# Kernel optimization log

Measured on AMD Instinct MI355X. Metric: run time of the kernel, lower is better.

The kernel has to match this reference:

```python
import jax, jax.numpy as jnp
import numpy as np

IMG = 64
STEPS = 10
UNITS = 256
PATCH_DIM = (IMG // 2) * (IMG // 2) * 9  # 3x3 patches, stride 2, SAME
ENC_IN = PATCH_DIM + 2 * UNITS  # read_window (patch+h_dec) concat h_dec again


def lstm_cell(x, h, c, kernel, rec, bias):
    # Keras LSTMCell gate order: i, f, g(candidate), o
    z = x @ kernel + h @ rec + bias
    i, f, g, o = jnp.split(z, 4, axis=-1)
    c_new = jax.nn.sigmoid(f) * c + jax.nn.sigmoid(i) * jnp.tanh(g)
    h_new = jax.nn.sigmoid(o) * jnp.tanh(c_new)
    return h_new, c_new


def extract_patches(img):
    # img: [B, H, W] -> 3x3 patches, stride 2, SAME -> [B, (H/2)*(W/2)*9]
    p = jax.lax.conv_general_dilated_patches(
        img[:, None, :, :], (3, 3), (2, 2), 'SAME')  # [B, 9, H/2, W/2]
    p = jnp.transpose(p, (0, 2, 3, 1))  # TF extract_patches layout [B,H',W',9]
    return p.reshape(img.shape[0], -1)


def setup_inputs() -> dict:
    key = jax.random.key(0)
    ks = jax.random.split(key, 8)
    B = 512
    s = 0.05  # small init scale to avoid gate saturation
    return {
        'x': jax.random.uniform(ks[0], (B, IMG, IMG), dtype=jnp.float32),
        'enc_kernel': jax.random.normal(ks[1], (ENC_IN, 4 * UNITS), dtype=jnp.float32) * s,
        'enc_rec': jax.random.normal(ks[2], (UNITS, 4 * UNITS), dtype=jnp.float32) * s,
        'enc_bias': jnp.zeros((4 * UNITS,), jnp.float32),
        'dec_kernel': jax.random.normal(ks[3], (UNITS, 4 * UNITS), dtype=jnp.float32) * s,
        'dec_rec': jax.random.normal(ks[4], (UNITS, 4 * UNITS), dtype=jnp.float32) * s,
        'dec_bias': jnp.zeros((4 * UNITS,), jnp.float32),
        'W_enc': jax.random.normal(ks[5], (UNITS, 10), dtype=jnp.float32) * s,
        'b_enc': jnp.zeros((10,), jnp.float32),
        'W_dec': jax.random.normal(ks[6], (UNITS, IMG * IMG), dtype=jnp.float32) * s,
        'b_dec': jnp.zeros((IMG * IMG,), jnp.float32),
    }


def reference(x, enc_kernel, enc_rec, enc_bias, dec_kernel, dec_rec, dec_bias,
              W_enc, b_enc, W_dec, b_dec):
    B = x.shape[0]
    canvas0 = jnp.zeros((B, IMG, IMG), x.dtype)
    h_enc0 = c_enc0 = h_dec0 = c_dec0 = jnp.zeros((B, UNITS), x.dtype)

    def step(carry, _):
        canvas, h_enc, c_enc, h_dec, c_dec = carry
        x_hat = x - jax.nn.sigmoid(canvas)                      # error image
        patches = extract_patches(x_hat)                        # [B, PATCH_DIM]
        read_window = jnp.concatenate([patches, h_dec], axis=1)
        enc_in = jnp.concatenate([read_window, h_dec], axis=1)  # [B, ENC_IN]
        h_enc, c_enc = lstm_cell(enc_in, h_enc, c_enc, enc_kernel, enc_rec, enc_bias)
        # attention over 10 slots; glimpse vector as attn-weighted slot embeddings
        attn = jax.nn.softmax(h_enc @ W_enc + b_enc, axis=1)    # [B, 10]
        z = attn @ W_enc.T                                      # [B, UNITS]
        h_dec, c_dec = lstm_cell(z, h_dec, c_dec, dec_kernel, dec_rec, dec_bias)
        canvas = canvas + (h_dec @ W_dec + b_dec).reshape(B, IMG, IMG)
        return (canvas, h_enc, c_enc, h_dec, c_dec), None

    (canvas, _, _, _, _), _ = jax.lax.scan(
        step, (canvas0, h_enc0, c_enc0, h_dec0, c_dec0), None, length=STEPS)
    return canvas
```

## Files before the change

### kernel.cpp

```cpp
#include <hip/hip_runtime.h>

typedef unsigned short ushort_t;
typedef __attribute__((ext_vector_type(8))) short short8;
typedef __attribute__((ext_vector_type(4))) float floatx4;

#define BSZ   512
#define UNITS 256
#define IMG   64
#define STEPS 10
#define GATES 1024
#define KENC  4608
#define ESPLIT 8
#define DSPLIT 4

__device__ inline float b2f(ushort_t u) {
  union { float f; unsigned int i; } v; v.i = ((unsigned int)u) << 16; return v.f;
}
__device__ inline ushort_t f2b(float f) {
  unsigned int u = __float_as_uint(f);
  u += 0x7fffu + ((u >> 16) & 1u);
  return (ushort_t)(u >> 16);
}
__device__ inline float sigm(float x) { return 1.f / (1.f + __expf(-x)); }

#define GLL(g, l) __builtin_amdgcn_global_load_lds(                      \
    (const __attribute__((address_space(1))) void*)(g),                  \
    (__attribute__((address_space(3))) void*)(l), 16, 0, 0)

__global__ __launch_bounds__(256) void k_prep_pix(const float* __restrict__ ek,
                                                  ushort_t* __restrict__ ohi) {
  __shared__ float T[64][68];
  int t = threadIdx.x;
  int pix0 = blockIdx.x * 64, n0 = blockIdx.y * 64;
  int r = t >> 2, seg = t & 3;
  int pix = pix0 + r;
  int ri = pix >> 6, ci = pix & 63;
  float4 acc4[4];
#pragma unroll
  for (int j = 0; j < 4; ++j) acc4[j] = float4{0.f, 0.f, 0.f, 0.f};
#pragma unroll
  for (int di = 0; di < 3; ++di) {
    int ii = ri - di;
    if (ii < 0 || (ii & 1)) continue;
    int oi = ii >> 1;  if (oi >= 32) continue;
#pragma unroll
    for (int dj = 0; dj < 3; ++dj) {
      int jj = ci - dj;
      if (jj < 0 || (jj & 1)) continue;
      int oj = jj >> 1;  if (oj >= 32) continue;
      const float* row = ek + (size_t)((oi * 32 + oj) * 9 + di * 3 + dj) * GATES
                         + n0 + seg * 16;
#pragma unroll
      for (int j = 0; j < 4; ++j) {
        float4 v = *(const float4*)(row + j * 4);
        acc4[j].x += v.x; acc4[j].y += v.y; acc4[j].z += v.z; acc4[j].w += v.w;
      }
    }
  }
#pragma unroll
  for (int j = 0; j < 4; ++j) *(float4*)&T[r][seg * 16 + j * 4] = acc4[j];
  __syncthreads();
  ushort_t thi[16];
#pragma unroll
  for (int j = 0; j < 16; ++j) thi[j] = f2b(T[seg * 16 + j][r]);
  size_t off = (size_t)(n0 + r) * KENC + pix0 + seg * 16;
  *(uint4*)(ohi + off)     = *(const uint4*)&thi[0];
  *(uint4*)(ohi + off + 8) = *(const uint4*)&thi[8];
}

__global__ __launch_bounds__(256) void k_prep_multi(
    const float* __restrict__ ek, const float* __restrict__ er,
    const float* __restrict__ dk, const float* __restrict__ dr,
    const float* __restrict__ Wdec,
    ushort_t* __restrict__ Wet_hi,
    ushort_t* __restrict__ Wdt_hi, ushort_t* __restrict__ Wdt_lo,
    ushort_t* __restrict__ Wct_hi, ushort_t* __restrict__ Wct_lo) {
  __shared__ float T[64][68];
  int t = threadIdx.x;
  int z = blockIdx.z;
  int k0 = blockIdx.x * 64, n0 = blockIdx.y * 64;
  int r = t >> 2, seg = t & 3;

  const float *s0, *s1 = nullptr;
  ushort_t *ohi, *olo = nullptr;
  int src_ld, out_ld, koff;
  if (z == 0) { s0 = ek + (size_t)9216 * GATES; s1 = ek + (size_t)9472 * GATES;
                src_ld = GATES; ohi = Wet_hi; out_ld = KENC; koff = 4096; }
  else if (z == 1) { s0 = er; src_ld = GATES; ohi = Wet_hi; out_ld = KENC; koff = 4352; }
  else if (z == 2) { s0 = dk; src_ld = GATES; ohi = Wdt_hi; olo = Wdt_lo; out_ld = 512; koff = 0; }
  else if (z == 3) { s0 = dr; src_ld = GATES; ohi = Wdt_hi; olo = Wdt_lo; out_ld = 512; koff = 256; }
  else { s0 = Wdec; src_ld = 4096; ohi = Wct_hi; olo = Wct_lo; out_ld = 256; koff = 0;
         n0 += (z - 4) * 1024; }

  const float* src = s0 + (size_t)(k0 + r) * src_ld + n0 + seg * 16;
  const float* src2 = s1 ? (s1 + (size_t)(k0 + r) * src_ld + n0 + seg * 16) : nullptr;
#pragma unroll
  for (int j = 0; j < 4; ++j) {
    float4 v = *(const float4*)(src + j * 4);
    if (src2) {
      float4 w = *(const float4*)(src2 + j * 4);
      v.x += w.x; v.y += w.y; v.z += w.z; v.w += w.w;
    }
    *(float4*)&T[r][seg * 16 + j * 4] = v;
  }
  __syncthreads();
  ushort_t thi[16], tlo[16];
#pragma unroll
  for (int j = 0; j < 16; ++j) {
    float v = T[seg * 16 + j][r];
    ushort_t h = f2b(v);
    thi[j] = h;
    tlo[j] = f2b(v - b2f(h));
  }
  size_t off = (size_t)(n0 + r) * out_ld + koff + k0 + seg * 16;
  *(uint4*)(ohi + off)     = *(const uint4*)&thi[0];
  *(uint4*)(ohi + off + 8) = *(const uint4*)&thi[8];
  if (olo) {
    *(uint4*)(olo + off)     = *(const uint4*)&tlo[0];
    *(uint4*)(olo + off + 8) = *(const uint4*)&tlo[8];
  }
}

__global__ __launch_bounds__(256) void k_init(float* __restrict__ canvas,
                                              float* __restrict__ c_enc,
                                              float* __restrict__ c_dec,
                                              ushort_t* __restrict__ ehi,
                                              ushort_t* __restrict__ dhi,
                                              ushort_t* __restrict__ dlo) {
  int b = blockIdx.x, u = threadIdx.x;
  int gid = b * 256 + u;
  float4* cv4 = (float4*)canvas;
#pragma unroll
  for (int j = 0; j < 4; ++j) cv4[gid + j * 131072] = float4{0.f, 0.f, 0.f, 0.f};
  c_enc[gid] = 0.f; c_dec[gid] = 0.f;
  ehi[(size_t)b * KENC + 4096 + u] = 0; ehi[(size_t)b * KENC + 4352 + u] = 0;
  dhi[(size_t)b * 512 + u] = 0; dhi[(size_t)b * 512 + 256 + u] = 0;
  dlo[(size_t)b * 512 + u] = 0; dlo[(size_t)b * 512 + 256 + u] = 0;
}

__global__ __launch_bounds__(256) void k_xhat0(const float* __restrict__ x,
                                               ushort_t* __restrict__ ehi) {
  int tid = blockIdx.x * 256 + threadIdx.x;
  int b = tid >> 12, pix = tid & 4095;
  ehi[(size_t)b * KENC + pix] = f2b(x[tid] - 0.5f);
}

#define TM 128
#define TN 128
#define BK 32

__global__ __launch_bounds__(512, 2) void gemm_e1(
    const ushort_t* __restrict__ Ahi, int lda,
    const ushort_t* __restrict__ Bhi, int ldbt,
    float* __restrict__ C, int ldc, int kiters) {
  __shared__ ushort_t ls[2][2][TM * BK];
  int t = threadIdx.x;
  int m0 = blockIdx.y * TM, n0 = blockIdx.x * TN;
  int z = blockIdx.z;
  int kstart = z * kiters * BK;
  int lane = t & 63, w = t >> 6;
  int wm = w >> 1, wn = w & 1;
  int q = lane >> 4, c16 = lane & 15;

  const ushort_t* pAh = Ahi + (size_t)(m0 + (t >> 2)) * lda + kstart + (t & 3) * 8;
  const ushort_t* pBh = Bhi + (size_t)(n0 + (t >> 2)) * ldbt + kstart + (t & 3) * 8;
  const int d0 = t * 8;

  floatx4 acc[2][4];
#pragma unroll
  for (int i = 0; i < 2; ++i)
#pragma unroll
    for (int j = 0; j < 4; ++j) acc[i][j] = floatx4{0.f, 0.f, 0.f, 0.f};

  GLL(pAh, &ls[0][0][d0]); GLL(pBh, &ls[0][1][d0]);
  pAh += BK; pBh += BK;
  __syncthreads();

  for (int kt = 0; kt < kiters; ++kt) {
    int cur = kt & 1, nxt = cur ^ 1;
    if (kt + 1 < kiters) {
      GLL(pAh, &ls[nxt][0][d0]); GLL(pBh, &ls[nxt][1][d0]);
      pAh += BK; pBh += BK;
    }
    short8 ah[2], bh[4];
#pragma unroll
    for (int i = 0; i < 2; ++i) {
      int ra = (wm * 32 + i * 16 + c16) * BK + q * 8;
      ah[i] = *(const short8*)&ls[cur][0][ra];
    }
#pragma unroll
    for (int j = 0; j < 4; ++j) {
      int rb = (wn * 64 + j * 16 + c16) * BK + q * 8;
      bh[j] = *(const short8*)&ls[cur][1][rb];
    }
#pragma unroll
    for (int mi = 0; mi < 2; ++mi)
#pragma unroll
      for (int ni = 0; ni < 4; ++ni)
        acc[mi][ni] = __builtin_amdgcn_mfma_f32_16x16x32_bf16(ah[mi], bh[ni], acc[mi][ni], 0, 0, 0);
    __syncthreads();
  }

  float* Cz = C + (size_t)z * BSZ * ldc;
#pragma unroll
  for (int mi = 0; mi < 2; ++mi)
#pragma unroll
    for (int ni = 0; ni < 4; ++ni) {
      int n = n0 + wn * 64 + ni * 16 + c16;
      int mb = m0 + wm * 32 + mi * 16 + q * 4;
#pragma unroll
      for (int r = 0; r < 4; ++r)
        Cz[(size_t)(mb + r) * ldc + n] = acc[mi][ni][r];
    }
}

__global__ __launch_bounds__(512, 2) void gemm_d(
    const ushort_t* __restrict__ Ahi, const ushort_t* __restrict__ Alo, int lda,
    const ushort_t* __restrict__ Bhi, const ushort_t* __restrict__ Blo, int ldbt,
    float* __restrict__ C, int ldc, int kiters) {
  __shared__ ushort_t ls[2][12288];
  int t = threadIdx.x;
  int m0 = blockIdx.y * TM, n0 = blockIdx.x * 64;
  int z = blockIdx.z;
  int kstart = z * kiters * BK;
  int lane = t & 63, w = t >> 6;
  int wm = w >> 1, wn = w & 1;
  int q = lane >> 4, c16 = lane & 15;
  int ta = t & 255;

  const ushort_t* pAh = Ahi + (size_t)(m0 + (t >> 2)) * lda + kstart + (t & 3) * 8;
  const ushort_t* pAl = Alo + (size_t)(m0 + (t >> 2)) * lda + kstart + (t & 3) * 8;
  const ushort_t* pB = ((t < 256) ? Bhi : Blo)
                       + (size_t)(n0 + (ta >> 2)) * ldbt + kstart + (ta & 3) * 8;
  const int dAh = t * 8, dAl = 4096 + t * 8;
  const int dB = ((t < 256) ? 8192 : 10240) + ta * 8;

  floatx4 acc[2][2];
#pragma unroll
  for (int i = 0; i < 2; ++i)
#pragma unroll
    for (int j = 0; j < 2; ++j) acc[i][j] = floatx4{0.f, 0.f, 0.f, 0.f};

  GLL(pAh, &ls[0][dAh]); GLL(pAl, &ls[0][dAl]); GLL(pB, &ls[0][dB]);
  pAh += BK; pAl += BK; pB += BK;
  __syncthreads();

  for (int kt = 0; kt < kiters; ++kt) {
    int cur = kt & 1, nxt = cur ^ 1;
    if (kt + 1 < kiters) {
      GLL(pAh, &ls[nxt][dAh]); GLL(pAl, &ls[nxt][dAl]); GLL(pB, &ls[nxt][dB]);
      pAh += BK; pAl += BK; pB += BK;
    }
    short8 ah[2], al[2], bh[2], bl[2];
#pragma unroll
    for (int i = 0; i < 2; ++i) {
      int ra = (wm * 32 + i * 16 + c16) * BK + q * 8;
      ah[i] = *(const short8*)&ls[cur][ra];
      al[i] = *(const short8*)&ls[cur][4096 + ra];
      int rb = (wn * 32 + i * 16 + c16) * BK + q * 8;
      bh[i] = *(const short8*)&ls[cur][8192 + rb];
      bl[i] = *(const short8*)&ls[cur][10240 + rb];
    }
#pragma unroll
    for (int mi = 0; mi < 2; ++mi)
#pragma unroll
      for (int ni = 0; ni < 2; ++ni) {
        acc[mi][ni] = __builtin_amdgcn_mfma_f32_16x16x32_bf16(ah[mi], bh[ni], acc[mi][ni], 0, 0, 0);
        acc[mi][ni] = __builtin_amdgcn_mfma_f32_16x16x32_bf16(ah[mi], bl[ni], acc[mi][ni], 0, 0, 0);
        acc[mi][ni] = __builtin_amdgcn_mfma_f32_16x16x32_bf16(al[mi], bh[ni], acc[mi][ni], 0, 0, 0);
      }
    __syncthreads();
  }

  float* Cz = C + (size_t)z * BSZ * ldc;
#pragma unroll
  for (int mi = 0; mi < 2; ++mi)
#pragma unroll
    for (int ni = 0; ni < 2; ++ni) {
      int n = n0 + wn * 32 + ni * 16 + c16;
      int mb = m0 + wm * 32 + mi * 16 + q * 4;
#pragma unroll
      for (int r = 0; r < 4; ++r)
        Cz[(size_t)(mb + r) * ldc + n] = acc[mi][ni][r];
    }
}

__global__ __launch_bounds__(256, 2) void gemm_cv(
    const ushort_t* __restrict__ Ahi, const ushort_t* __restrict__ Alo, int lda,
    const ushort_t* __restrict__ Bhi, const ushort_t* __restrict__ Blo, int ldbt,
    float* __restrict__ canvas, const float* __restrict__ x,
    const float* __restrict__ bdec, ushort_t* __restrict__ ehi) {
  __shared__ ushort_t ls[2][4][TM * BK];
  int t = threadIdx.x;
  int m0 = blockIdx.y * TM, n0 = blockIdx.x * TN;
  int lane = t & 63, w = t >> 6;
  int wm = w >> 1, wn = w & 1;
  int q = lane >> 4, c16 = lane & 15;
  const int kiters = 8;

  const ushort_t* pAh = Ahi + (size_t)(m0 + (t >> 2)) * lda + (t & 3) * 8;
  const ushort_t* pAl = Alo + (size_t)(m0 + (t >> 2)) * lda + (t & 3) * 8;
  const ushort_t* pBh = Bhi + (size_t)(n0 + (t >> 2)) * ldbt + (t & 3) * 8;
  const ushort_t* pBl = Blo + (size_t)(n0 + (t >> 2)) * ldbt + (t & 3) * 8;
  const size_t a64 = (size_t)64 * lda, b64 = (size_t)64 * ldbt;
  const int d0 = t * 8;

  floatx4 acc[4][4];
#pragma unroll
  for (int i = 0; i < 4; ++i)
#pragma unroll
    for (int j = 0; j < 4; ++j) acc[i][j] = floatx4{0.f, 0.f, 0.f, 0.f};

  GLL(pAh, &ls[0][0][d0]); GLL(pAh + a64, &ls[0][0][d0 + 2048]);
  GLL(pAl, &ls[0][1][d0]); GLL(pAl + a64, &ls[0][1][d0 + 2048]);
  GLL(pBh, &ls[0][2][d0]); GLL(pBh + b64, &ls[0][2][d0 + 2048]);
  GLL(pBl, &ls[0][3][d0]); GLL(pBl + b64, &ls[0][3][d0 + 2048]);
  pAh += BK; pAl += BK; pBh += BK; pBl += BK;
  __syncthreads();

  for (int kt = 0; kt < kiters; ++kt) {
    int cur = kt & 1, nxt = cur ^ 1;
    if (kt + 1 < kiters) {
      GLL(pAh, &ls[nxt][0][d0]); GLL(pAh + a64, &ls[nxt][0][d0 + 2048]);
      GLL(pAl, &ls[nxt][1][d0]); GLL(pAl + a64, &ls[nxt][1][d0 + 2048]);
      GLL(pBh, &ls[nxt][2][d0]); GLL(pBh + b64, &ls[nxt][2][d0 + 2048]);
      GLL(pBl, &ls[nxt][3][d0]); GLL(pBl + b64, &ls[nxt][3][d0 + 2048]);
      pAh += BK; pAl += BK; pBh += BK; pBl += BK;
    }
    short8 ah[4], al[4], bh[4], bl[4];
#pragma unroll
    for (int i = 0; i < 4; ++i) {
      int ra = (wm * 64 + i * 16 + c16) * BK + q * 8;
      int rb = (wn * 64 + i * 16 + c16) * BK + q * 8;
      ah[i] = *(const short8*)&ls[cur][0][ra];
      al[i] = *(const short8*)&ls[cur][1][ra];
      bh[i] = *(const short8*)&ls[cur][2][rb];
      bl[i] = *(const short8*)&ls[cur][3][rb];
    }
#pragma unroll
    for (int mi = 0; mi < 4; ++mi)
#pragma unroll
      for (int ni = 0; ni < 4; ++ni) {
        acc[mi][ni] = __builtin_amdgcn_mfma_f32_16x16x32_bf16(ah[mi], bh[ni], acc[mi][ni], 0, 0, 0);
        acc[mi][ni] = __builtin_amdgcn_mfma_f32_16x16x32_bf16(ah[mi], bl[ni], acc[mi][ni], 0, 0, 0);
        acc[mi][ni] = __builtin_amdgcn_mfma_f32_16x16x32_bf16(al[mi], bh[ni], acc[mi][ni], 0, 0, 0);
      }
    __syncthreads();
  }

#pragma unroll
  for (int mi = 0; mi < 4; ++mi)
#pragma unroll
    for (int ni = 0; ni < 4; ++ni) {
      int n = n0 + wn * 64 + ni * 16 + c16;
      int mb = m0 + wm * 64 + mi * 16 + q * 4;
      float bv = bdec[n];
#pragma unroll
      for (int r = 0; r < 4; ++r) {
        int m = mb + r;
        size_t idx = (size_t)m * 4096 + n;
        float cv = canvas[idx] + acc[mi][ni][r] + bv;
        canvas[idx] = cv;
        float xh = x[idx] - sigm(cv);
        ehi[(size_t)m * KENC + n] = f2b(xh);
      }
    }
}

__global__ __launch_bounds__(256) void k_enc(const float* __restrict__ zparts, int S,
                                             const float* __restrict__ ebias,
                                             float* __restrict__ c_enc,
                                             ushort_t* __restrict__ ehi,
                                             const float* __restrict__ Wenc,
                                             const float* __restrict__ benc,
                                             ushort_t* __restrict__ dhi,
                                             ushort_t* __restrict__ dlo) {
  int b = blockIdx.x, u = threadIdx.x;
  float zi = ebias[u],       zf = ebias[u + 256];
  float zg = ebias[u + 512], zo = ebias[u + 768];
  for (int s = 0; s < S; ++s) {
    const float* z = zparts + ((size_t)s * BSZ + b) * GATES;
    zi += z[u]; zf += z[u + 256]; zg += z[u + 512]; zo += z[u + 768];
  }
  float c = c_enc[b * UNITS + u];
  float cn = sigm(zf) * c + sigm(zi) * tanhf(zg);
  float h = sigm(zo) * tanhf(cn);
  c_enc[b * UNITS + u] = cn;
  ehi[(size_t)b * KENC + 4352 + u] = f2b(h);

  __shared__ float sh[UNITS];
  __shared__ float slog[10];
  sh[u] = h;
  __syncthreads();
  if (u < 64) {
    float acc[10];
#pragma unroll
    for (int j = 0; j < 10; ++j) acc[j] = 0.f;
    for (int qq = 0; qq < 4; ++qq) {
      float hv = sh[u + qq * 64];
      const float* wr = Wenc + (u + qq * 64) * 10;
#pragma unroll
      for (int j = 0; j < 10; ++j) acc[j] += hv * wr[j];
    }
    for (int off = 32; off > 0; off >>= 1)
#pragma unroll
      for (int j = 0; j < 10; ++j) acc[j] += __shfl_down(acc[j], off);
    if (u == 0)
      for (int j = 0; j < 10; ++j) slog[j] = acc[j] + benc[j];
  }
  __syncthreads();
  float mx = slog[0];
  for (int j = 1; j < 10; ++j) mx = fmaxf(mx, slog[j]);
  float e[10], se = 0.f;
  for (int j = 0; j < 10; ++j) { e[j] = __expf(slog[j] - mx); se += e[j]; }
  float inv = 1.f / se;
  const float* wr = Wenc + u * 10;
  float zz = 0.f;
  for (int j = 0; j < 10; ++j) zz += e[j] * inv * wr[j];
  ushort_t zh = f2b(zz);
  dhi[(size_t)b * 512 + u] = zh;
  dlo[(size_t)b * 512 + u] = f2b(zz - b2f(zh));
}

__global__ __launch_bounds__(256) void k_dec(const float* __restrict__ zparts, int S,
                                             const float* __restrict__ dbias,
                                             float* __restrict__ c_dec,
                                             ushort_t* __restrict__ dhi,
                                             ushort_t* __restrict__ dlo,
                                             ushort_t* __restrict__ ehi) {
  int b = blockIdx.x, u = threadIdx.x;
  float zi = dbias[u],       zf = dbias[u + 256];
  float zg = dbias[u + 512], zo = dbias[u + 768];
  for (int s = 0; s < S; ++s) {
    const float* z = zparts + ((size_t)s * BSZ + b) * GATES;
    zi += z[u]; zf += z[u + 256]; zg += z[u + 512]; zo += z[u + 768];
  }
  float c = c_dec[b * UNITS + u];
  float cn = sigm(zf) * c + sigm(zi) * tanhf(zg);
  float h = sigm(zo) * tanhf(cn);
  c_dec[b * UNITS + u] = cn;
  ushort_t hh = f2b(h);
  dhi[(size_t)b * 512 + 256 + u] = hh;
  dlo[(size_t)b * 512 + 256 + u] = f2b(h - b2f(hh));
  ehi[(size_t)b * KENC + 4096 + u] = hh;
}

extern "C" void kernel_launch(void* const* d_in, const int* in_sizes, int n_in,
                              void* d_out, int out_size, void* d_ws, size_t ws_size,
                              hipStream_t stream) {
  const float* x     = (const float*)d_in[0];
  const float* ek    = (const float*)d_in[1];
  const float* er    = (const float*)d_in[2];
  const float* ebias = (const float*)d_in[3];
  const float* dk    = (const float*)d_in[4];
  const float* dr    = (const float*)d_in[5];
  const float* dbias = (const float*)d_in[6];
  const float* Wenc  = (const float*)d_in[7];
  const float* benc  = (const float*)d_in[8];
  const float* Wdec  = (const float*)d_in[9];
  const float* bdec  = (const float*)d_in[10];

  float* canvas = (float*)d_out;

  char* p = (char*)d_ws;
  float* c_enc  = (float*)p;        p += (size_t)BSZ * UNITS * 4;
  float* c_dec  = (float*)p;        p += (size_t)BSZ * UNITS * 4;
  float* zep    = (float*)p;        p += (size_t)ESPLIT * BSZ * GATES * 4;
  float* zdp    = (float*)p;        p += (size_t)DSPLIT * BSZ * GATES * 4;
  ushort_t* ehi = (ushort_t*)p;     p += (size_t)BSZ * KENC * 2;
  ushort_t* dhi = (ushort_t*)p;     p += (size_t)BSZ * 512 * 2;
  ushort_t* dlo = (ushort_t*)p;     p += (size_t)BSZ * 512 * 2;
  ushort_t* Wet_hi = (ushort_t*)p;  p += (size_t)GATES * KENC * 2;
  ushort_t* Wdt_hi = (ushort_t*)p;  p += (size_t)GATES * 512 * 2;
  ushort_t* Wdt_lo = (ushort_t*)p;  p += (size_t)GATES * 512 * 2;
  ushort_t* Wct_hi = (ushort_t*)p;  p += (size_t)4096 * UNITS * 2;
  ushort_t* Wct_lo = (ushort_t*)p;  p += (size_t)4096 * UNITS * 2;

  k_prep_pix<<<dim3(64, 16), 256, 0, stream>>>(ek, Wet_hi);
  k_prep_multi<<<dim3(4, 16, 8), 256, 0, stream>>>(ek, er, dk, dr, Wdec,
                                                   Wet_hi, Wdt_hi, Wdt_lo,
                                                   Wct_hi, Wct_lo);
  k_init<<<BSZ, 256, 0, stream>>>(canvas, c_enc, c_dec, ehi, dhi, dlo);
  k_xhat0<<<(BSZ * 4096) / 256, 256, 0, stream>>>(x, ehi);

  for (int s = 0; s < STEPS; ++s) {
    gemm_e1<<<dim3(GATES / 128, BSZ / 128, ESPLIT), 512, 0, stream>>>(
        ehi, KENC, Wet_hi, KENC, zep, GATES, 18);
    k_enc<<<BSZ, 256, 0, stream>>>(zep, ESPLIT, ebias, c_enc, ehi, Wenc, benc, dhi, dlo);
    gemm_d<<<dim3(GATES / 64, BSZ / 128, DSPLIT), 512, 0, stream>>>(
        dhi, dlo, 512, Wdt_hi, Wdt_lo, 512, zdp, GATES, 4);
    k_dec<<<BSZ, 256, 0, stream>>>(zdp, DSPLIT, dbias, c_dec, dhi, dlo, ehi);
    gemm_cv<<<dim3(4096 / 128, BSZ / 128), 256, 0, stream>>>(
        dhi + 256, dlo + 256, 512, Wct_hi, Wct_lo, 256, canvas, x, bdec, ehi);
  }
}
```

Baseline: 680.2 us.

## Fuse per-step kernels into one persistent cooperative kernel with grid barriers

Replaces the 5 kernel launches per step (plus the init kernels) with a single persistent kernel of 256 blocks. A hand-rolled atomic grid barrier separates the encoder GEMM, encoder cell, decoder GEMM, decoder cell and canvas GEMM phases. The aim is to remove launch overhead and inter-kernel gaps across 10 steps. The canvas GEMM is retiled to 64x128 so it fits 256 blocks, which lowers per-block reuse. The software barrier costs spin-wait time and relies on every block being co-resident, which the non-cooperative fallback launch does not guarantee.

```diff
diff --git a/kernel.cpp b/kernel.cpp
--- a/kernel.cpp
+++ b/kernel.cpp
@@ -12,6 +12,10 @@
 #define KENC  4608
 #define ESPLIT 8
 #define DSPLIT 4
+#define NBLK  256
+#define TM 128
+#define TN 128
+#define BK 32
 
 __device__ inline float b2f(ushort_t u) {
   union { float f; unsigned int i; } v; v.i = ((unsigned int)u) << 16; return v.f;
@@ -26,6 +30,26 @@
 #define GLL(g, l) __builtin_amdgcn_global_load_lds(                      \
     (const __attribute__((address_space(1))) void*)(g),                  \
     (__attribute__((address_space(3))) void*)(l), 16, 0, 0)
+
+__device__ inline void gridbar(unsigned* bar) {
+  __syncthreads();
+  if (threadIdx.x == 0) {
+    __threadfence();
+    unsigned* cnt = bar;
+    unsigned* gen = bar + 1;
+    unsigned g = __hip_atomic_load(gen, __ATOMIC_RELAXED, __HIP_MEMORY_SCOPE_AGENT);
+    unsigned a = __hip_atomic_fetch_add(cnt, 1u, __ATOMIC_ACQ_REL, __HIP_MEMORY_SCOPE_AGENT);
+    if (a == NBLK - 1) {
+      __hip_atomic_store(cnt, 0u, __ATOMIC_RELAXED, __HIP_MEMORY_SCOPE_AGENT);
+      __hip_atomic_store(gen, g + 1u, __ATOMIC_RELEASE, __HIP_MEMORY_SCOPE_AGENT);
+    } else {
+      while (__hip_atomic_load(gen, __ATOMIC_ACQUIRE, __HIP_MEMORY_SCOPE_AGENT) == g)
+        __builtin_amdgcn_s_sleep(1);
+    }
+    __threadfence();
+  }
+  __syncthreads();
+}
 
 __global__ __launch_bounds__(256) void k_prep_pix(const float* __restrict__ ek,
                                                   ushort_t* __restrict__ ohi) {
@@ -74,12 +98,16 @@
     const float* __restrict__ Wdec,
     ushort_t* __restrict__ Wet_hi,
     ushort_t* __restrict__ Wdt_hi, ushort_t* __restrict__ Wdt_lo,
-    ushort_t* __restrict__ Wct_hi, ushort_t* __restrict__ Wct_lo) {
+    ushort_t* __restrict__ Wct_hi, ushort_t* __restrict__ Wct_lo,
+    unsigned* __restrict__ bar) {
   __shared__ float T[64][68];
   int t = threadIdx.x;
   int z = blockIdx.z;
   int k0 = blockIdx.x * 64, n0 = blockIdx.y * 64;
   int r = t >> 2, seg = t & 3;
+  if (z == 0 && blockIdx.x == 0 && blockIdx.y == 0 && t == 0) {
+    bar[0] = 0u; bar[1] = 0u;
+  }
 
   const float *s0, *s1 = nullptr;
   ushort_t *ohi, *olo = nullptr;
@@ -121,328 +149,284 @@
   }
 }
 
-__global__ __launch_bounds__(256) void k_init(float* __restrict__ canvas,
-                                              float* __restrict__ c_enc,
-                                              float* __restrict__ c_dec,
-                                              ushort_t* __restrict__ ehi,
-                                              ushort_t* __restrict__ dhi,
-                                              ushort_t* __restrict__ dlo) {
-  int b = blockIdx.x, u = threadIdx.x;
-  int gid = b * 256 + u;
-  float4* cv4 = (float4*)canvas;
-#pragma unroll
-  for (int j = 0; j < 4; ++j) cv4[gid + j * 131072] = float4{0.f, 0.f, 0.f, 0.f};
-  c_enc[gid] = 0.f; c_dec[gid] = 0.f;
-  ehi[(size_t)b * KENC + 4096 + u] = 0; ehi[(size_t)b * KENC + 4352 + u] = 0;
-  dhi[(size_t)b * 512 + u] = 0; dhi[(size_t)b * 512 + 256 + u] = 0;
-  dlo[(size_t)b * 512 + u] = 0; dlo[(size_t)b * 512 + 256 + u] = 0;
-}
-
-__global__ __launch_bounds__(256) void k_xhat0(const float* __restrict__ x,
-                                               ushort_t* __restrict__ ehi) {
-  int tid = blockIdx.x * 256 + threadIdx.x;
-  int b = tid >> 12, pix = tid & 4095;
-  ehi[(size_t)b * KENC + pix] = f2b(x[tid] - 0.5f);
-}
-
-#define TM 128
-#define TN 128
-#define BK 32
-
-__global__ __launch_bounds__(512, 2) void gemm_e1(
-    const ushort_t* __restrict__ Ahi, int lda,
-    const ushort_t* __restrict__ Bhi, int ldbt,
-    float* __restrict__ C, int ldc, int kiters) {
-  __shared__ ushort_t ls[2][2][TM * BK];
-  int t = threadIdx.x;
-  int m0 = blockIdx.y * TM, n0 = blockIdx.x * TN;
-  int z = blockIdx.z;
-  int kstart = z * kiters * BK;
-  int lane = t & 63, w = t >> 6;
-  int wm = w >> 1, wn = w & 1;
-  int q = lane >> 4, c16 = lane & 15;
-
-  const ushort_t* pAh = Ahi + (size_t)(m0 + (t >> 2)) * lda + kstart + (t & 3) * 8;
-  const ushort_t* pBh = Bhi + (size_t)(n0 + (t >> 2)) * ldbt + kstart + (t & 3) * 8;
-  const int d0 = t * 8;
-
-  floatx4 acc[2][4];
-#pragma unroll
-  for (int i = 0; i < 2; ++i)
-#pragma unroll
-    for (int j = 0; j < 4; ++j) acc[i][j] = floatx4{0.f, 0.f, 0.f, 0.f};
-
-  GLL(pAh, &ls[0][0][d0]); GLL(pBh, &ls[0][1][d0]);
-  pAh += BK; pBh += BK;
-  __syncthreads();
-
-  for (int kt = 0; kt < kiters; ++kt) {
-    int cur = kt & 1, nxt = cur ^ 1;
-    if (kt + 1 < kiters) {
-      GLL(pAh, &ls[nxt][0][d0]); GLL(pBh, &ls[nxt][1][d0]);
+__global__ __launch_bounds__(512, 2) void k_persist(
+    const float* __restrict__ x,
+    const float* __restrict__ ebias, const float* __restrict__ dbias,
+    const float* __restrict__ Wenc, const float* __restrict__ benc,
+    const float* __restrict__ bdec,
+    float* __restrict__ canvas, float* __restrict__ c_enc, float* __restrict__ c_dec,
+    float* __restrict__ zep, float* __restrict__ zdp,
+    ushort_t* __restrict__ ehi, ushort_t* __restrict__ dhi, ushort_t* __restrict__ dlo,
+    const ushort_t* __restrict__ Wet_hi,
+    const ushort_t* __restrict__ Wdt_hi, const ushort_t* __restrict__ Wdt_lo,
+    const ushort_t* __restrict__ Wct_hi, const ushort_t* __restrict__ Wct_lo,
+    unsigned* bar) {
+  __shared__ __align__(16) ushort_t smem[24576];
+  const int b = blockIdx.x, t = threadIdx.x;
+  const int lane = t & 63, w = t >> 6;
+  const int q = lane >> 4, c16 = lane & 15;
+  const int half = t >> 8, u8 = t & 255;
+  const int rrow = b * 2 + half;
+
+  {
+    float4* cv4 = (float4*)canvas;
+    float4 z4 = float4{0.f, 0.f, 0.f, 0.f};
+#pragma unroll
+    for (int i = 0; i < 4; ++i) cv4[b * 2048 + i * 512 + t] = z4;
+    c_enc[b * 512 + t] = 0.f;
+    c_dec[b * 512 + t] = 0.f;
+    ehi[(size_t)rrow * KENC + 4096 + u8] = 0;
+    ehi[(size_t)rrow * KENC + 4352 + u8] = 0;
+    dhi[(size_t)rrow * 512 + u8] = 0; dhi[(size_t)rrow * 512 + 256 + u8] = 0;
+    dlo[(size_t)rrow * 512 + u8] = 0; dlo[(size_t)rrow * 512 + 256 + u8] = 0;
+    for (int pix = u8; pix < 4096; pix += 256)
+      ehi[(size_t)rrow * KENC + pix] = f2b(x[(size_t)rrow * 4096 + pix] - 0.5f);
+  }
+  gridbar(bar);
+
+  for (int s = 0; s < STEPS; ++s) {
+    {
+      const int z = b >> 5, by = (b >> 3) & 3, bx = b & 7;
+      const int m0 = by * TM, n0 = bx * TN, kstart = z * 18 * BK;
+      const int wm = w >> 1, wn = w & 1;
+      const ushort_t* pAh = ehi + (size_t)(m0 + (t >> 2)) * KENC + kstart + (t & 3) * 8;
+      const ushort_t* pBh = Wet_hi + (size_t)(n0 + (t >> 2)) * KENC + kstart + (t & 3) * 8;
+      const int d0 = t * 8;
+
+      floatx4 acc[2][4];
+#pragma unroll
+      for (int i = 0; i < 2; ++i)
+#pragma unroll
+        for (int j = 0; j < 4; ++j) acc[i][j] = floatx4{0.f, 0.f, 0.f, 0.f};
+
+      GLL(pAh, &smem[d0]); GLL(pBh, &smem[4096 + d0]);
       pAh += BK; pBh += BK;
-    }
-    short8 ah[2], bh[4];
-#pragma unroll
-    for (int i = 0; i < 2; ++i) {
-      int ra = (wm * 32 + i * 16 + c16) * BK + q * 8;
-      ah[i] = *(const short8*)&ls[cur][0][ra];
-    }
-#pragma unroll
-    for (int j = 0; j < 4; ++j) {
-      int rb = (wn * 64 + j * 16 + c16) * BK + q * 8;
-      bh[j] = *(const short8*)&ls[cur][1][rb];
-    }
-#pragma unroll
-    for (int mi = 0; mi < 2; ++mi)
-#pragma unroll
-      for (int ni = 0; ni < 4; ++ni)
-        acc[mi][ni] = __builtin_amdgcn_mfma_f32_16x16x32_bf16(ah[mi], bh[ni], acc[mi][ni], 0, 0, 0);
-    __syncthreads();
-  }
-
-  float* Cz = C + (size_t)z * BSZ * ldc;
-#pragma unroll
-  for (int mi = 0; mi < 2; ++mi)
-#pragma unroll
-    for (int ni = 0; ni < 4; ++ni) {
-      int n = n0 + wn * 64 + ni * 16 + c16;
-      int mb = m0 + wm * 32 + mi * 16 + q * 4;
-#pragma unroll
-      for (int r = 0; r < 4; ++r)
-        Cz[(size_t)(mb + r) * ldc + n] = acc[mi][ni][r];
-    }
-}
-
-__global__ __launch_bounds__(512, 2) void gemm_d(
-    const ushort_t* __restrict__ Ahi, const ushort_t* __restrict__ Alo, int lda,
-    const ushort_t* __restrict__ Bhi, const ushort_t* __restrict__ Blo, int ldbt,
-    float* __restrict__ C, int ldc, int kiters) {
-  __shared__ ushort_t ls[2][12288];
-  int t = threadIdx.x;
-  int m0 = blockIdx.y * TM, n0 = blockIdx.x * 64;
-  int z = blockIdx.z;
-  int kstart = z * kiters * BK;
-  int lane = t & 63, w = t >> 6;
-  int wm = w >> 1, wn = w & 1;
-  int q = lane >> 4, c16 = lane & 15;
-  int ta = t & 255;
-
-  const ushort_t* pAh = Ahi + (size_t)(m0 + (t >> 2)) * lda + kstart + (t & 3) * 8;
-  const ushort_t* pAl = Alo + (size_t)(m0 + (t >> 2)) * lda + kstart + (t & 3) * 8;
-  const ushort_t* pB = ((t < 256) ? Bhi : Blo)
-                       + (size_t)(n0 + (ta >> 2)) * ldbt + kstart + (ta & 3) * 8;
-  const int dAh = t * 8, dAl = 4096 + t * 8;
-  const int dB = ((t < 256) ? 8192 : 10240) + ta * 8;
-
-  floatx4 acc[2][2];
-#pragma unroll
-  for (int i = 0; i < 2; ++i)
-#pragma unroll
-    for (int j = 0; j < 2; ++j) acc[i][j] = floatx4{0.f, 0.f, 0.f, 0.f};
-
-  GLL(pAh, &ls[0][dAh]); GLL(pAl, &ls[0][dAl]); GLL(pB, &ls[0][dB]);
-  pAh += BK; pAl += BK; pB += BK;
-  __syncthreads();
-
-  for (int kt = 0; kt < kiters; ++kt) {
-    int cur = kt & 1, nxt = cur ^ 1;
-    if (kt + 1 < kiters) {
-      GLL(pAh, &ls[nxt][dAh]); GLL(pAl, &ls[nxt][dAl]); GLL(pB, &ls[nxt][dB]);
+      __syncthreads();
+      for (int kt = 0; kt < 18; ++kt) {
+        const int cur = (kt & 1) * 8192, nxt = 8192 - cur;
+        if (kt + 1 < 18) {
+          GLL(pAh, &smem[nxt + d0]); GLL(pBh, &smem[nxt + 4096 + d0]);
+          pAh += BK; pBh += BK;
+        }
+        short8 ah[2], bh[4];
+#pragma unroll
+        for (int i = 0; i < 2; ++i)
+          ah[i] = *(const short8*)&smem[cur + (wm * 32 + i * 16 + c16) * BK + q * 8];
+#pragma unroll
+        for (int j = 0; j < 4; ++j)
+          bh[j] = *(const short8*)&smem[cur + 4096 + (wn * 64 + j * 16 + c16) * BK + q * 8];
+#pragma unroll
+        for (int mi = 0; mi < 2; ++mi)
+#pragma unroll
+          for (int ni = 0; ni < 4; ++ni)
+            acc[mi][ni] = __builtin_amdgcn_mfma_f32_16x16x32_bf16(ah[mi], bh[ni], acc[mi][ni], 0, 0, 0);
+        __syncthreads();
+      }
+      float* Cz = zep + (size_t)z * BSZ * GATES;
+#pragma unroll
+      for (int mi = 0; mi < 2; ++mi)
+#pragma unroll
+        for (int ni = 0; ni < 4; ++ni) {
+          const int n = n0 + wn * 64 + ni * 16 + c16;
+          const int mb = m0 + wm * 32 + mi * 16 + q * 4;
+#pragma unroll
+          for (int r = 0; r < 4; ++r)
+            Cz[(size_t)(mb + r) * GATES + n] = acc[mi][ni][r];
+        }
+    }
+    gridbar(bar);
+
+    {
+      float* shf = (float*)smem;
+      float zi = ebias[u8], zf = ebias[u8 + 256];
+      float zg = ebias[u8 + 512], zo = ebias[u8 + 768];
+      for (int sp = 0; sp < ESPLIT; ++sp) {
+        const float* zz = zep + ((size_t)sp * BSZ + rrow) * GATES;
+        zi += zz[u8]; zf += zz[u8 + 256]; zg += zz[u8 + 512]; zo += zz[u8 + 768];
+      }
+      float c = c_enc[rrow * UNITS + u8];
+      float cn = sigm(zf) * c + sigm(zi) * tanhf(zg);
+      float h = sigm(zo) * tanhf(cn);
+      c_enc[rrow * UNITS + u8] = cn;
+      ehi[(size_t)rrow * KENC + 4352 + u8] = f2b(h);
+      shf[half * 256 + u8] = h;
+      __syncthreads();
+      if (u8 < 64) {
+        float acc[10];
+#pragma unroll
+        for (int j = 0; j < 10; ++j) acc[j] = 0.f;
+        for (int qq = 0; qq < 4; ++qq) {
+          float hv = shf[half * 256 + u8 + qq * 64];
+          const float* wr = Wenc + (u8 + qq * 64) * 10;
+#pragma unroll
+          for (int j = 0; j < 10; ++j) acc[j] += hv * wr[j];
+        }
+        for (int off = 32; off > 0; off >>= 1)
+#pragma unroll
+          for (int j = 0; j < 10; ++j) acc[j] += __shfl_down(acc[j], off);
+        if (u8 == 0)
+          for (int j = 0; j < 10; ++j) shf[512 + half * 10 + j] = acc[j] + benc[j];
+      }
+      __syncthreads();
+      float mx = shf[512 + half * 10];
+      for (int j = 1; j < 10; ++j) mx = fmaxf(mx, shf[512 + half * 10 + j]);
+      float e[10], se = 0.f;
+      for (int j = 0; j < 10; ++j) { e[j] = __expf(shf[512 + half * 10 + j] - mx); se += e[j]; }
+      float inv = 1.f / se;
+      const float* wr = Wenc + u8 * 10;
+      float zzv = 0.f;
+      for (int j = 0; j < 10; ++j) zzv += e[j] * inv * wr[j];
+      ushort_t zh = f2b(zzv);
+      dhi[(size_t)rrow * 512 + u8] = zh;
+      dlo[(size_t)rrow * 512 + u8] = f2b(zzv - b2f(zh));
+    }
+    gridbar(bar);
+
+    {
+      const int z = b >> 6, rem = b & 63, by = rem >> 4, bx = rem & 15;
+      const int m0 = by * TM, n0 = bx * 64, kstart = z * 4 * BK;
+      const int wm = w >> 1, wn = w & 1;
+      const int ta = t & 255;
+      const ushort_t* pAh = dhi + (size_t)(m0 + (t >> 2)) * 512 + kstart + (t & 3) * 8;
+      const ushort_t* pAl = dlo + (size_t)(m0 + (t >> 2)) * 512 + kstart + (t & 3) * 8;
+      const ushort_t* pB = ((t < 256) ? Wdt_hi : Wdt_lo)
+                           + (size_t)(n0 + (ta >> 2)) * 512 + kstart + (ta & 3) * 8;
+      const int dAh = t * 8, dAl = 4096 + t * 8;
+      const int dB = ((t < 256) ? 8192 : 10240) + ta * 8;
+
+      floatx4 acc[2][2];
+#pragma unroll
+      for (int i = 0; i < 2; ++i)
+#pragma unroll
+        for (int j = 0; j < 2; ++j) acc[i][j] = floatx4{0.f, 0.f, 0.f, 0.f};
+
+      GLL(pAh, &smem[dAh]); GLL(pAl, &smem[dAl]); GLL(pB, &smem[dB]);
       pAh += BK; pAl += BK; pB += BK;
-    }
-    short8 ah[2], al[2], bh[2], bl[2];
-#pragma unroll
-    for (int i = 0; i < 2; ++i) {
-      int ra = (wm * 32 + i * 16 + c16) * BK + q * 8;
-      ah[i] = *(const short8*)&ls[cur][ra];
-      al[i] = *(const short8*)&ls[cur][4096 + ra];
-      int rb = (wn * 32 + i * 16 + c16) * BK + q * 8;
-      bh[i] = *(const short8*)&ls[cur][8192 + rb];
-      bl[i] = *(const short8*)&ls[cur][10240 + rb];
-    }
-#pragma unroll
-    for (int mi = 0; mi < 2; ++mi)
-#pragma unroll
-      for (int ni = 0; ni < 2; ++ni) {
-        acc[mi][ni] = __builtin_amdgcn_mfma_f32_16x16x32_bf16(ah[mi], bh[ni], acc[mi][ni], 0, 0, 0);
-        acc[mi][ni] = __builtin_amdgcn_mfma_f32_16x16x32_bf16(ah[mi], bl[ni], acc[mi][ni], 0, 0, 0);
-        acc[mi][ni] = __builtin_amdgcn_mfma_f32_16x16x32_bf16(al[mi], bh[ni], acc[mi][ni], 0, 0, 0);
-      }
-    __syncthreads();
-  }
-
-  float* Cz = C + (size_t)z * BSZ * ldc;
-#pragma unroll
-  for (int mi = 0; mi < 2; ++mi)
-#pragma unroll
-    for (int ni = 0; ni < 2; ++ni) {
-      int n = n0 + wn * 32 + ni * 16 + c16;
-      int mb = m0 + wm * 32 + mi * 16 + q * 4;
-#pragma unroll
-      for (int r = 0; r < 4; ++r)
-        Cz[(size_t)(mb + r) * ldc + n] = acc[mi][ni][r];
-    }
-}
-
-__global__ __launch_bounds__(256, 2) void gemm_cv(
-    const ushort_t* __restrict__ Ahi, const ushort_t* __restrict__ Alo, int lda,
-    const ushort_t* __restrict__ Bhi, const ushort_t* __restrict__ Blo, int ldbt,
-    float* __restrict__ canvas, const float* __restrict__ x,
-    const float* __restrict__ bdec, ushort_t* __restrict__ ehi) {
-  __shared__ ushort_t ls[2][4][TM * BK];
-  int t = threadIdx.x;
-  int m0 = blockIdx.y * TM, n0 = blockIdx.x * TN;
-  int lane = t & 63, w = t >> 6;
-  int wm = w >> 1, wn = w & 1;
-  int q = lane >> 4, c16 = lane & 15;
-  const int kiters = 8;
-
-  const ushort_t* pAh = Ahi + (size_t)(m0 + (t >> 2)) * lda + (t & 3) * 8;
-  const ushort_t* pAl = Alo + (size_t)(m0 + (t >> 2)) * lda + (t & 3) * 8;
-  const ushort_t* pBh = Bhi + (size_t)(n0 + (t >> 2)) * ldbt + (t & 3) * 8;
-  const ushort_t* pBl = Blo + (size_t)(n0 + (t >> 2)) * ldbt + (t & 3) * 8;
-  const size_t a64 = (size_t)64 * lda, b64 = (size_t)64 * ldbt;
-  const int d0 = t * 8;
-
-  floatx4 acc[4][4];
-#pragma unroll
-  for (int i = 0; i < 4; ++i)
-#pragma unroll
-    for (int j = 0; j < 4; ++j) acc[i][j] = floatx4{0.f, 0.f, 0.f, 0.f};
-
-  GLL(pAh, &ls[0][0][d0]); GLL(pAh + a64, &ls[0][0][d0 + 2048]);
-  GLL(pAl, &ls[0][1][d0]); GLL(pAl + a64, &ls[0][1][d0 + 2048]);
-  GLL(pBh, &ls[0][2][d0]); GLL(pBh + b64, &ls[0][2][d0 + 2048]);
-  GLL(pBl, &ls[0][3][d0]); GLL(pBl + b64, &ls[0][3][d0 + 2048]);
-  pAh += BK; pAl += BK; pBh += BK; pBl += BK;
-  __syncthreads();
-
-  for (int kt = 0; kt < kiters; ++kt) {
-    int cur = kt & 1, nxt = cur ^ 1;
-    if (kt + 1 < kiters) {
-      GLL(pAh, &ls[nxt][0][d0]); GLL(pAh + a64, &ls[nxt][0][d0 + 2048]);
-      GLL(pAl, &ls[nxt][1][d0]); GLL(pAl + a64, &ls[nxt][1][d0 + 2048]);
-      GLL(pBh, &ls[nxt][2][d0]); GLL(pBh + b64, &ls[nxt][2][d0 + 2048]);
-      GLL(pBl, &ls[nxt][3][d0]); GLL(pBl + b64, &ls[nxt][3][d0 + 2048]);
-      pAh += BK; pAl += BK; pBh += BK; pBl += BK;
-    }
-    short8 ah[4], al[4], bh[4], bl[4];
-#pragma unroll
-    for (int i = 0; i < 4; ++i) {
-      int ra = (wm * 64 + i * 16 + c16) * BK + q * 8;
-      int rb = (wn * 64 + i * 16 + c16) * BK + q * 8;
-      ah[i] = *(const short8*)&ls[cur][0][ra];
-      al[i] = *(const short8*)&ls[cur][1][ra];
-      bh[i] = *(const short8*)&ls[cur][2][rb];
-      bl[i] = *(const short8*)&ls[cur][3][rb];
-    }
-#pragma unroll
-    for (int mi = 0; mi < 4; ++mi)
-#pragma unroll
-      for (int ni = 0; ni < 4; ++ni) {
-        acc[mi][ni] = __builtin_amdgcn_mfma_f32_16x16x32_bf16(ah[mi], bh[ni], acc[mi][ni], 0, 0, 0);
-        acc[mi][ni] = __builtin_amdgcn_mfma_f32_16x16x32_bf16(ah[mi], bl[ni], acc[mi][ni], 0, 0, 0);
-        acc[mi][ni] = __builtin_amdgcn_mfma_f32_16x16x32_bf16(al[mi], bh[ni], acc[mi][ni], 0, 0, 0);
-      }
-    __syncthreads();
-  }
-
-#pragma unroll
-  for (int mi = 0; mi < 4; ++mi)
-#pragma unroll
-    for (int ni = 0; ni < 4; ++ni) {
-      int n = n0 + wn * 64 + ni * 16 + c16;
-      int mb = m0 + wm * 64 + mi * 16 + q * 4;
-      float bv = bdec[n];
-#pragma unroll
-      for (int r = 0; r < 4; ++r) {
-        int m = mb + r;
-        size_t idx = (size_t)m * 4096 + n;
-        float cv = canvas[idx] + acc[mi][ni][r] + bv;
-        canvas[idx] = cv;
-        float xh = x[idx] - sigm(cv);
-        ehi[(size_t)m * KENC + n] = f2b(xh);
-      }
-    }
-}
-
-__global__ __launch_bounds__(256) void k_enc(const float* __restrict__ zparts, int S,
-                                             const float* __restrict__ ebias,
-                                             float* __restrict__ c_enc,
-                                             ushort_t* __restrict__ ehi,
-                                             const float* __restrict__ Wenc,
-                                             const float* __restrict__ benc,
-                                             ushort_t* __restrict__ dhi,
-                                             ushort_t* __restrict__ dlo) {
-  int b = blockIdx.x, u = threadIdx.x;
-  float zi = ebias[u],       zf = ebias[u + 256];
-  float zg = ebias[u + 512], zo = ebias[u + 768];
-  for (int s = 0; s < S; ++s) {
-    const float* z = zparts + ((size_t)s * BSZ + b) * GATES;
-    zi += z[u]; zf += z[u + 256]; zg += z[u + 512]; zo += z[u + 768];
-  }
-  float c = c_enc[b * UNITS + u];
-  float cn = sigm(zf) * c + sigm(zi) * tanhf(zg);
-  float h = sigm(zo) * tanhf(cn);
-  c_enc[b * UNITS + u] = cn;
-  ehi[(size_t)b * KENC + 4352 + u] = f2b(h);
-
-  __shared__ float sh[UNITS];
-  __shared__ float slog[10];
-  sh[u] = h;
-  __syncthreads();
-  if (u < 64) {
-    float acc[10];
-#pragma unroll
-    for (int j = 0; j < 10; ++j) acc[j] = 0.f;
-    for (int qq = 0; qq < 4; ++qq) {
-      float hv = sh[u + qq * 64];
-      const float* wr = Wenc + (u + qq * 64) * 10;
-#pragma unroll
-      for (int j = 0; j < 10; ++j) acc[j] += hv * wr[j];
-    }
-    for (int off = 32; off > 0; off >>= 1)
-#pragma unroll
-      for (int j = 0; j < 10; ++j) acc[j] += __shfl_down(acc[j], off);
-    if (u == 0)
-      for (int j = 0; j < 10; ++j) slog[j] = acc[j] + benc[j];
-  }
-  __syncthreads();
-  float mx = slog[0];
-  for (int j = 1; j < 10; ++j) mx = fmaxf(mx, slog[j]);
-  float e[10], se = 0.f;
-  for (int j = 0; j < 10; ++j) { e[j] = __expf(slog[j] - mx); se += e[j]; }
-  float inv = 1.f / se;
-  const float* wr = Wenc + u * 10;
-  float zz = 0.f;
-  for (int j = 0; j < 10; ++j) zz += e[j] * inv * wr[j];
-  ushort_t zh = f2b(zz);
-  dhi[(size_t)b * 512 + u] = zh;
-  dlo[(size_t)b * 512 + u] = f2b(zz - b2f(zh));
-}
-
-__global__ __launch_bounds__(256) void k_dec(const float* __restrict__ zparts, int S,
-                                             const float* __restrict__ dbias,
-                                             float* __restrict__ c_dec,
-                                             ushort_t* __restrict__ dhi,
-                                             ushort_t* __restrict__ dlo,
-                                             ushort_t* __restrict__ ehi) {
-  int b = blockIdx.x, u = threadIdx.x;
-  float zi = dbias[u],       zf = dbias[u + 256];
-  float zg = dbias[u + 512], zo = dbias[u + 768];
-  for (int s = 0; s < S; ++s) {
-    const float* z = zparts + ((size_t)s * BSZ + b) * GATES;
-    zi += z[u]; zf += z[u + 256]; zg += z[u + 512]; zo += z[u + 768];
-  }
-  float c = c_dec[b * UNITS + u];
-  float cn = sigm(zf) * c + sigm(zi) * tanhf(zg);
-  float h = sigm(zo) * tanhf(cn);
-  c_dec[b * UNITS + u] = cn;
-  ushort_t hh = f2b(h);
-  dhi[(size_t)b * 512 + 256 + u] = hh;
-  dlo[(size_t)b * 512 + 256 + u] = f2b(h - b2f(hh));
-  ehi[(size_t)b * KENC + 4096 + u] = hh;
+      __syncthreads();
+      for (int kt = 0; kt < 4; ++kt) {
+        const int cur = (kt & 1) * 12288, nxt = 12288 - cur;
+        if (kt + 1 < 4) {
+          GLL(pAh, &smem[nxt + dAh]); GLL(pAl, &smem[nxt + dAl]); GLL(pB, &smem[nxt + dB]);
+          pAh += BK; pAl += BK; pB += BK;
+        }
+        short8 ah[2], al[2], bh[2], bl[2];
+#pragma unroll
+        for (int i = 0; i < 2; ++i) {
+          const int ra = (wm * 32 + i * 16 + c16) * BK + q * 8;
+          ah[i] = *(const short8*)&smem[cur + ra];
+          al[i] = *(const short8*)&smem[cur + 4096 + ra];
+          const int rb = (wn * 32 + i * 16 + c16) * BK + q * 8;
+          bh[i] = *(const short8*)&smem[cur + 8192 + rb];
+          bl[i] = *(const short8*)&smem[cur + 10240 + rb];
+        }
+#pragma unroll
+        for (int mi = 0; mi < 2; ++mi)
+#pragma unroll
+          for (int ni = 0; ni < 2; ++ni) {
+            acc[mi][ni] = __builtin_amdgcn_mfma_f32_16x16x32_bf16(ah[mi], bh[ni], acc[mi][ni], 0, 0, 0);
+            acc[mi][ni] = __builtin_amdgcn_mfma_f32_16x16x32_bf16(ah[mi], bl[ni], acc[mi][ni], 0, 0, 0);
+            acc[mi][ni] = __builtin_amdgcn_mfma_f32_16x16x32_bf16(al[mi], bh[ni], acc[mi][ni], 0, 0, 0);
+          }
+        __syncthreads();
+      }
+      float* Cz = zdp + (size_t)z * BSZ * GATES;
+#pragma unroll
+      for (int mi = 0; mi < 2; ++mi)
+#pragma unroll
+        for (int ni = 0; ni < 2; ++ni) {
+          const int n = n0 + wn * 32 + ni * 16 + c16;
+          const int mb = m0 + wm * 32 + mi * 16 + q * 4;
+#pragma unroll
+          for (int r = 0; r < 4; ++r)
+            Cz[(size_t)(mb + r) * GATES + n] = acc[mi][ni][r];
+        }
+    }
+    gridbar(bar);
+
+    {
+      float zi = dbias[u8], zf = dbias[u8 + 256];
+      float zg = dbias[u8 + 512], zo = dbias[u8 + 768];
+      for (int sp = 0; sp < DSPLIT; ++sp) {
+        const float* zz = zdp + ((size_t)sp * BSZ + rrow) * GATES;
+        zi += zz[u8]; zf += zz[u8 + 256]; zg += zz[u8 + 512]; zo += zz[u8 + 768];
+      }
+      float c = c_dec[rrow * UNITS + u8];
+      float cn = sigm(zf) * c + sigm(zi) * tanhf(zg);
+      float h = sigm(zo) * tanhf(cn);
+      c_dec[rrow * UNITS + u8] = cn;
+      ushort_t hh = f2b(h);
+      dhi[(size_t)rrow * 512 + 256 + u8] = hh;
+      dlo[(size_t)rrow * 512 + 256 + u8] = f2b(h - b2f(hh));
+      ehi[(size_t)rrow * KENC + 4096 + u8] = hh;
+    }
+    gridbar(bar);
+
+    {
+      const int by = b >> 5, bx = b & 31;
+      const int m0 = by * 64, n0 = bx * TN;
+      const int wm = w >> 2, wn = w & 3;
+      const int ia = t & 255;
+      const ushort_t* pA = ((t < 256) ? (dhi + 256) : (dlo + 256))
+                           + (size_t)(m0 + (ia >> 2)) * 512 + (ia & 3) * 8;
+      const ushort_t* pBh = Wct_hi + (size_t)(n0 + (t >> 2)) * 256 + (t & 3) * 8;
+      const ushort_t* pBl = Wct_lo + (size_t)(n0 + (t >> 2)) * 256 + (t & 3) * 8;
+      const int dA = ((t < 256) ? 0 : 2048) + ia * 8;
+      const int dBh = 4096 + t * 8, dBl = 8192 + t * 8;
+
+      floatx4 acc[2][2];
+#pragma unroll
+      for (int i = 0; i < 2; ++i)
+#pragma unroll
+        for (int j = 0; j < 2; ++j) acc[i][j] = floatx4{0.f, 0.f, 0.f, 0.f};
+
+      GLL(pA, &smem[dA]); GLL(pBh, &smem[dBh]); GLL(pBl, &smem[dBl]);
+      pA += BK; pBh += BK; pBl += BK;
+      __syncthreads();
+      for (int kt = 0; kt < 8; ++kt) {
+        const int cur = (kt & 1) * 12288, nxt = 12288 - cur;
+        if (kt + 1 < 8) {
+          GLL(pA, &smem[nxt + dA]); GLL(pBh, &smem[nxt + dBh]); GLL(pBl, &smem[nxt + dBl]);
+          pA += BK; pBh += BK; pBl += BK;
+        }
+        short8 ah[2], al[2], bh[2], bl[2];
+#pragma unroll
+        for (int i = 0; i < 2; ++i) {
+          const int ra = (wm * 32 + i * 16 + c16) * BK + q * 8;
+          ah[i] = *(const short8*)&smem[cur + ra];
+          al[i] = *(const short8*)&smem[cur + 2048 + ra];
+          const int rb = (wn * 32 + i * 16 + c16) * BK + q * 8;
+          bh[i] = *(const short8*)&smem[cur + 4096 + rb];
+          bl[i] = *(const short8*)&smem[cur + 8192 + rb];
+        }
+#pragma unroll
+        for (int mi = 0; mi < 2; ++mi)
+#pragma unroll
+          for (int ni = 0; ni < 2; ++ni) {
+            acc[mi][ni] = __builtin_amdgcn_mfma_f32_16x16x32_bf16(ah[mi], bh[ni], acc[mi][ni], 0, 0, 0);
+            acc[mi][ni] = __builtin_amdgcn_mfma_f32_16x16x32_bf16(ah[mi], bl[ni], acc[mi][ni], 0, 0, 0);
+            acc[mi][ni] = __builtin_amdgcn_mfma_f32_16x16x32_bf16(al[mi], bh[ni], acc[mi][ni], 0, 0, 0);
+          }
+        __syncthreads();
+      }
+#pragma unroll
+      for (int mi = 0; mi < 2; ++mi)
+#pragma unroll
+        for (int ni = 0; ni < 2; ++ni) {
+          const int n = n0 + wn * 32 + ni * 16 + c16;
+          const int mb = m0 + wm * 32 + mi * 16 + q * 4;
+          const float bv = bdec[n];
+#pragma unroll
+          for (int r = 0; r < 4; ++r) {
+            const int m = mb + r;
+            const size_t idx = (size_t)m * 4096 + n;
+            const float cv = canvas[idx] + acc[mi][ni][r] + bv;
+            canvas[idx] = cv;
+            ehi[(size_t)m * KENC + n] = f2b(x[idx] - sigm(cv));
+          }
+        }
+    }
+    if (s + 1 < STEPS) gridbar(bar);
+  }
 }
 
 extern "C" void kernel_launch(void* const* d_in, const int* in_sizes, int n_in,
@@ -475,22 +459,22 @@
   ushort_t* Wdt_lo = (ushort_t*)p;  p += (size_t)GATES * 512 * 2;
   ushort_t* Wct_hi = (ushort_t*)p;  p += (size_t)4096 * UNITS * 2;
   ushort_t* Wct_lo = (ushort_t*)p;  p += (size_t)4096 * UNITS * 2;
+  unsigned* bar = (unsigned*)p;     p += 8;
 
   k_prep_pix<<<dim3(64, 16), 256, 0, stream>>>(ek, Wet_hi);
   k_prep_multi<<<dim3(4, 16, 8), 256, 0, stream>>>(ek, er, dk, dr, Wdec,
                                                    Wet_hi, Wdt_hi, Wdt_lo,
-                                                   Wct_hi, Wct_lo);
-  k_init<<<BSZ, 256, 0, stream>>>(canvas, c_enc, c_dec, ehi, dhi, dlo);
-  k_xhat0<<<(BSZ * 4096) / 256, 256, 0, stream>>>(x, ehi);
-
-  for (int s = 0; s < STEPS; ++s) {
-    gemm_e1<<<dim3(GATES / 128, BSZ / 128, ESPLIT), 512, 0, stream>>>(
-        ehi, KENC, Wet_hi, KENC, zep, GATES, 18);
-    k_enc<<<BSZ, 256, 0, stream>>>(zep, ESPLIT, ebias, c_enc, ehi, Wenc, benc, dhi, dlo);
-    gemm_d<<<dim3(GATES / 64, BSZ / 128, DSPLIT), 512, 0, stream>>>(
-        dhi, dlo, 512, Wdt_hi, Wdt_lo, 512, zdp, GATES, 4);
-    k_dec<<<BSZ, 256, 0, stream>>>(zdp, DSPLIT, dbias, c_dec, dhi, dlo, ehi);
-    gemm_cv<<<dim3(4096 / 128, BSZ / 128), 256, 0, stream>>>(
-        dhi + 256, dlo + 256, 512, Wct_hi, Wct_lo, 256, canvas, x, bdec, ehi);
-  }
-}
+                                                   Wct_hi, Wct_lo, bar);
+
+  void* args[] = {(void*)&x, (void*)&ebias, (void*)&dbias, (void*)&Wenc,
+                  (void*)&benc, (void*)&bdec, (void*)&canvas, (void*)&c_enc,
+                  (void*)&c_dec, (void*)&zep, (void*)&zdp, (void*)&ehi,
+                  (void*)&dhi, (void*)&dlo, (void*)&Wet_hi, (void*)&Wdt_hi,
+                  (void*)&Wdt_lo, (void*)&Wct_hi, (void*)&Wct_lo, (void*)&bar};
+  if (hipLaunchCooperativeKernel((void*)k_persist, dim3(NBLK), dim3(512),
+                                 args, 0, stream) != hipSuccess) {
+    k_persist<<<dim3(NBLK), dim3(512), 0, stream>>>(
+        x, ebias, dbias, Wenc, benc, bdec, canvas, c_enc, c_dec, zep, zdp,
+        ehi, dhi, dlo, Wet_hi, Wdt_hi, Wdt_lo, Wct_hi, Wct_lo, bar);
+  }
+}
```

New measurement: 2.609 ms. 3.84x slower.
